# Kernel optimization log

Hardware: AMD Instinct MI355X
Metric: run time of the kernel (lower is better)

The kernel has to match this reference:

```python
import jax, jax.numpy as jnp
import numpy as np

DIM = 512; NH = 8; HD = DIM // NH; WS = 28; N = WS * WS; H3 = (DIM * 4) // 3; EPS = 1e-6; B = 16


def _rel_pos_index(H, W):
    # static numpy computation of Swin-style relative position index [N, N]
    coords = np.stack(np.meshgrid(np.arange(H), np.arange(W), indexing='ij')).reshape(2, -1)
    rel = (coords[:, :, None] - coords[:, None, :]).transpose(1, 2, 0)
    rel[..., 0] += H - 1
    rel[..., 1] += W - 1
    rel[..., 0] *= 2 * W - 1
    return rel.sum(-1)

RPI = jnp.asarray(_rel_pos_index(WS, WS))  # [N, N] int


def adaptive_ln(x, w, b, a1w, a1b, a2w, a2b):
    # x: [B,C,H,W]; adapt params from global-avg-pooled 1x1 convs (== matmuls)
    C = x.shape[1]
    pooled = x.mean(axis=(2, 3))                      # [B,C]
    h = jax.nn.relu(pooled @ a1w.T + a1b)             # [B,C/4]
    ad = h @ a2w.T + a2b                              # [B,2C]
    aw = ad[:, :C][:, :, None, None]
    ab = ad[:, C:][:, :, None, None]
    u = x.mean(axis=1, keepdims=True)
    s = ((x - u) ** 2).mean(axis=1, keepdims=True)
    xn = (x - u) * jax.lax.rsqrt(s + EPS)
    return (w[None, :, None, None] * (1.0 + aw)) * xn + (b[None, :, None, None] + ab)


def dwconv(x, w, b):
    y = jax.lax.conv_general_dilated(x, w, (1, 1), 'SAME', feature_group_count=x.shape[1],
                                     dimension_numbers=('NCHW', 'OIHW', 'NCHW'))
    return y + b[None, :, None, None]


def conv1x1(x, w, b):
    return jnp.einsum('bchw,oc->bohw', x, w) + b[None, :, None, None]


def _forward(x, face_priors, n1_w, n1_b, n1_a1w, n1_a1b, n1_a2w, n1_a2b,
             n2_w, n2_b, n2_a1w, n2_a1b, n2_a2w, n2_a2b,
             qkv_w, qkv_b, rpb_table, struct_prior, proj_w, proj_b,
             eye_w, eye_b, nose_w, nose_b, mouth_w, mouth_b,
             fusion_w, fusion_b, gate1_w, gate1_b, gate2_w, gate2_b,
             es1_w, es1_b, es2_w, es2_b, em1_w, em1_b, em2_w, em2_b,
             el1_w, el1_b, el2_w, el2_b, router_w, router_b):
    Bx, C, H, W = x.shape
    n = H * W
    shortcut = x
    xa = adaptive_ln(x, n1_w, n1_b, n1_a1w, n1_a1b, n1_a2w, n1_a2b)
    # --- TripletFaceAttention ---
    xf = xa.reshape(Bx, C, n).transpose(0, 2, 1)                     # [B,N,C]
    qkv = (xf @ qkv_w.T + qkv_b).reshape(Bx, n, 3, NH, HD).transpose(2, 0, 3, 1, 4)
    q, k, v = qkv[0], qkv[1], qkv[2]                                 # [B,h,N,d]
    attn = jnp.einsum('bhnd,bhmd->bhnm', q, k) * (HD ** -0.5)
    attn = attn + struct_prior                                       # learned structure prior [1,h,N,N]
    rpb = rpb_table[RPI]                                             # [N,N,h]
    attn = attn + jnp.transpose(rpb, (2, 0, 1))[None]                # + relative position bias
    attn = attn * face_priors[:, None]                               # multiplicative face mask
    attn = jax.nn.softmax(attn, axis=-1)
    o = jnp.einsum('bhnm,bhmd->bhnd', attn, v).transpose(0, 2, 1, 3).reshape(Bx, n, C)
    o = o @ proj_w.T + proj_b
    x = shortcut + o.transpose(0, 2, 1).reshape(Bx, C, H, W)
    # --- FaceTokenMixer ---
    xn2 = adaptive_ln(x, n2_w, n2_b, n2_a1w, n2_a1b, n2_a2w, n2_a2b)
    cat = jnp.concatenate([dwconv(xn2, eye_w, eye_b),
                           dwconv(xn2, nose_w, nose_b),
                           dwconv(xn2, mouth_w, mouth_b)], axis=1)   # [B,3C,H,W]
    g = jax.nn.sigmoid(conv1x1(jax.nn.relu(conv1x1(xn2, gate1_w, gate1_b)), gate2_w, gate2_b))
    x = x + conv1x1(cat * g, fusion_w, fusion_b)
    # --- EfficientMLP (3-expert MoE, soft routing) ---
    r = jax.nn.softmax(x.mean(axis=(2, 3)) @ router_w.T + router_b, axis=-1)  # [B,3]
    def expert(w1, b1, w2, b2):
        return conv1x1(jax.nn.gelu(conv1x1(x, w1, b1), approximate=False), w2, b2)
    out = (r[:, 0, None, None, None] * expert(es1_w, es1_b, es2_w, es2_b)
           + r[:, 1, None, None, None] * expert(em1_w, em1_b, em2_w, em2_b)
           + r[:, 2, None, None, None] * expert(el1_w, el1_b, el2_w, el2_b))
    return x + out


def setup_inputs() -> dict:
    ks = iter(jax.random.split(jax.random.key(0), 64))
    def rn(shape, s=0.02):
        return jax.random.normal(next(ks), shape, jnp.float32) * s
    d = {}
    d['x'] = jax.random.normal(next(ks), (B, DIM, WS, WS), jnp.float32)
    d['face_priors'] = jax.random.uniform(next(ks), (B, N, N), jnp.float32)
    for p in ('n1', 'n2'):
        d[p + '_w'] = jnp.ones((DIM,), jnp.float32)
        d[p + '_b'] = jnp.zeros((DIM,), jnp.float32)
        d[p + '_a1w'] = rn((DIM // 4, DIM)); d[p + '_a1b'] = jnp.zeros((DIM // 4,), jnp.float32)
        d[p + '_a2w'] = rn((2 * DIM, DIM // 4)); d[p + '_a2b'] = jnp.zeros((2 * DIM,), jnp.float32)
    d['qkv_w'] = rn((3 * DIM, DIM)); d['qkv_b'] = jnp.zeros((3 * DIM,), jnp.float32)
    d['rpb_table'] = rn(((2 * WS - 1) ** 2, NH))
    d['struct_prior'] = rn((1, NH, N, N))
    d['proj_w'] = rn((DIM, DIM)); d['proj_b'] = jnp.zeros((DIM,), jnp.float32)
    d['eye_w'] = rn((DIM, 1, 3, 3)); d['eye_b'] = jnp.zeros((DIM,), jnp.float32)
    d['nose_w'] = rn((DIM, 1, 5, 5)); d['nose_b'] = jnp.zeros((DIM,), jnp.float32)
    d['mouth_w'] = rn((DIM, 1, 7, 7)); d['mouth_b'] = jnp.zeros((DIM,), jnp.float32)
    d['fusion_w'] = rn((DIM, 3 * DIM)); d['fusion_b'] = jnp.zeros((DIM,), jnp.float32)
    d['gate1_w'] = rn((DIM // 4, DIM)); d['gate1_b'] = jnp.zeros((DIM // 4,), jnp.float32)
    d['gate2_w'] = rn((3 * DIM, DIM // 4)); d['gate2_b'] = jnp.zeros((3 * DIM,), jnp.float32)
    for e in ('es', 'em', 'el'):
        d[e + '1_w'] = rn((H3, DIM)); d[e + '1_b'] = jnp.zeros((H3,), jnp.float32)
        d[e + '2_w'] = rn((DIM, H3)); d[e + '2_b'] = jnp.zeros((DIM,), jnp.float32)
    d['router_w'] = rn((3, DIM)); d['router_b'] = jnp.zeros((3,), jnp.float32)
    return d


def reference(x, face_priors, n1_w, n1_b, n1_a1w, n1_a1b, n1_a2w, n1_a2b,
              n2_w, n2_b, n2_a1w, n2_a1b, n2_a2w, n2_a2b,
              qkv_w, qkv_b, rpb_table, struct_prior, proj_w, proj_b,
              eye_w, eye_b, nose_w, nose_b, mouth_w, mouth_b,
              fusion_w, fusion_b, gate1_w, gate1_b, gate2_w, gate2_b,
              es1_w, es1_b, es2_w, es2_b, em1_w, em1_b, em2_w, em2_b,
              el1_w, el1_b, el2_w, el2_b, router_w, router_b):
    return _forward(x, face_priors, n1_w, n1_b, n1_a1w, n1_a1b, n1_a2w, n1_a2b,
                    n2_w, n2_b, n2_a1w, n2_a1b, n2_a2w, n2_a2b,
                    qkv_w, qkv_b, rpb_table, struct_prior, proj_w, proj_b,
                    eye_w, eye_b, nose_w, nose_b, mouth_w, mouth_b,
                    fusion_w, fusion_b, gate1_w, gate1_b, gate2_w, gate2_b,
                    es1_w, es1_b, es2_w, es2_b, em1_w, em1_b, em2_w, em2_b,
                    el1_w, el1_b, el2_w, el2_b, router_w, router_b)
```

## Files before the change

### kernel.cpp

```cpp
#include <hip/hip_runtime.h>
#include <math.h>


#define NPIX 784
#define CDIM 512
#define NHEAD 8
#define C3 1536

typedef unsigned int uint;
typedef unsigned short ushort;
typedef float f32x4 __attribute__((ext_vector_type(4)));
typedef __bf16 bf16x8 __attribute__((ext_vector_type(8)));
typedef __bf16 bf16x2 __attribute__((ext_vector_type(2)));

#define OFF_XPM ((size_t)0)
#define OFF_W   ((size_t)3211264)
#define OFF_R2  ((size_t)5324288)
#define OFF_VBF ((size_t)14958080)
#define OFF_OBF ((size_t)18169344)
#define OFF_X2  ((size_t)21380608)
#define OFF_X3  ((size_t)27803136)
#define OFF_PL  ((size_t)34225664)
#define OFF_AD  ((size_t)34233856)
#define OFF_RB  ((size_t)34250240)
#define OFF_US  ((size_t)34250288)
#define OFF_RS  ((size_t)34262832)
#define OFF_E2C ((size_t)34275392)

#define WOFF_QKV 0
#define WOFF_PROJ 786432
#define WOFF_G1  1048576
#define WOFF_G2  1114112
#define WOFF_FUS 1310720
#define WOFF_E1  2097152

__device__ __forceinline__ ushort f2bf(float f) {
  __bf16 h = (__bf16)f;
  return __builtin_bit_cast(ushort, h);
}
__device__ __forceinline__ unsigned pack2bf(float lo, float hi) {
  bf16x2 v = {(__bf16)lo, (__bf16)hi};
  return __builtin_bit_cast(unsigned, v);
}
__device__ __forceinline__ float bf2f(ushort u) {
  unsigned x = ((unsigned)u) << 16;
  return __builtin_bit_cast(float, x);
}
__device__ __forceinline__ void unpack4bf(uint2 v, float* o) {
  o[0] = bf2f((ushort)(v.x & 0xffffu)); o[1] = bf2f((ushort)(v.x >> 16));
  o[2] = bf2f((ushort)(v.y & 0xffffu)); o[3] = bf2f((ushort)(v.y >> 16));
}

__global__ __launch_bounds__(64) void pool_mean_k(const float* __restrict__ x,
                                                  float* __restrict__ pooled) {
  int c = blockIdx.x, b = blockIdx.y;
  const float* row = x + ((size_t)b * CDIM + c) * NPIX;
  float s = 0.f;
  for (int i = threadIdx.x; i < NPIX; i += 64) s += row[i];
  #pragma unroll
  for (int off = 32; off; off >>= 1) s += __shfl_down(s, off);
  if (threadIdx.x == 0) pooled[b * CDIM + c] = s;
}

__global__ __launch_bounds__(256) void adapt_mlp_k(const float* __restrict__ pooled,
                                                   const float* __restrict__ a1w,
                                                   const float* __restrict__ a1b,
                                                   const float* __restrict__ a2w,
                                                   const float* __restrict__ a2b,
                                                   float* __restrict__ ad) {
  int b = blockIdx.x, tid = threadIdx.x;
  __shared__ float pl[CDIM];
  __shared__ float hh[128];
  for (int i = tid; i < CDIM; i += 256)
    pl[i] = pooled[b * CDIM + i] * (1.f / NPIX);
  __syncthreads();
  if (tid < 128) {
    const float* w = a1w + (size_t)tid * CDIM;
    float a = a1b[tid];
    for (int k = 0; k < CDIM; ++k) a += w[k] * pl[k];
    hh[tid] = fmaxf(a, 0.f);
  }
  __syncthreads();
  for (int o = tid; o < 1024; o += 256) {
    const float* w = a2w + (size_t)o * 128;
    float a = a2b[o];
    for (int k = 0; k < 128; ++k) a += w[k] * hh[k];
    ad[b * 1024 + o] = a;
  }
}

template <int STATS>
__global__ __launch_bounds__(256) void ln_pm_k(const float* __restrict__ x,
                                               const float* __restrict__ w,
                                               const float* __restrict__ bias,
                                               const float* __restrict__ ad,
                                               ushort* __restrict__ out,
                                               float* __restrict__ ust,
                                               float* __restrict__ rstp) {
  int b = blockIdx.y;
  int p0 = blockIdx.x * 32;
  int tid = threadIdx.x;
  int px = tid & 31, cg = tid >> 5;
  int p = p0 + px;
  bool valid = p < NPIX;
  const float* xb = x + (size_t)b * CDIM * NPIX;
  float s = 0.f, s2 = 0.f;
  if (valid) {
    for (int c = cg * 64; c < cg * 64 + 64; ++c) {
      float v = xb[(size_t)c * NPIX + p];
      s += v; s2 += v * v;
    }
  }
  __shared__ float rs[8][32], rq[8][32], us[32], vs[32];
  rs[cg][px] = s; rq[cg][px] = s2;
  __syncthreads();
  if (tid < 32) {
    float ts = 0.f, ts2 = 0.f;
    #pragma unroll
    for (int g = 0; g < 8; ++g) { ts += rs[g][tid]; ts2 += rq[g][tid]; }
    float u = ts * (1.f / CDIM);
    float var = ts2 * (1.f / CDIM) - u * u;
    float rv = rsqrtf(var + 1e-6f);
    us[tid] = u; vs[tid] = rv;
    if (STATS && p0 + tid < NPIX) {
      ust[(size_t)b * NPIX + p0 + tid] = u;
      rstp[(size_t)b * NPIX + p0 + tid] = rv;
    }
  }
  __syncthreads();
  if (valid) {
    float u = us[px], rv = vs[px];
    const float* aw = ad + (size_t)b * 1024;
    const float* ab = aw + CDIM;
    ushort* ob = out + ((size_t)(b * NPIX + p)) * CDIM + cg * 64;
    for (int cb = 0; cb < 64; cb += 8) {
      int c = cg * 64 + cb;
      float vv[8];
      #pragma unroll
      for (int q = 0; q < 8; ++q) {
        float v = xb[(size_t)(c + q) * NPIX + p];
        vv[q] = w[c + q] * (1.f + aw[c + q]) * ((v - u) * rv) + (bias[c + q] + ab[c + q]);
      }
      uint4 o = {pack2bf(vv[0], vv[1]), pack2bf(vv[2], vv[3]),
                 pack2bf(vv[4], vv[5]), pack2bf(vv[6], vv[7])};
      *(uint4*)(ob + cb) = o;
    }
  }
}

struct CvtDesc {
  const float* s[11];
  ushort* d[11];
  int rows[11], sk[11], dk[11], ds[11], rr[11];
};
__global__ __launch_bounds__(256) void cvt_w_k(CvtDesc D) {
  int seg = blockIdx.y;
  int sk = D.sk[seg], dk = D.dk[seg], ds = D.ds[seg], rr = D.rr[seg];
  int total = D.rows[seg] * dk;
  const float* s = D.s[seg];
  ushort* d = D.d[seg];
  for (int i = blockIdx.x * 256 + threadIdx.x; i < total; i += gridDim.x * 256) {
    int r = i / dk, cc = i - r * dk;
    d[(size_t)r * ds + cc] = (cc < sk && r < rr) ? f2bf(s[(size_t)r * sk + cc]) : (ushort)0;
  }
}

__global__ __launch_bounds__(256) void sprpb_k(const float* __restrict__ sp,
                                               const float* __restrict__ rpb,
                                               ushort* __restrict__ out) {
  const int q = blockIdx.x, h = blockIdx.y;
  const int i1 = q / 28, j1 = q - i1 * 28;
  const float* src = sp + ((size_t)h * NPIX + q) * NPIX;
  ushort* dst = out + ((size_t)h * NPIX + q) * NPIX;
  for (int m = threadIdx.x; m < NPIX; m += 256) {
    int i2 = m / 28, j2 = m - i2 * 28;
    float rv = rpb[(size_t)((i1 - i2 + 27) * 55 + (j1 - j2 + 27)) * NHEAD + h];
    dst[m] = f2bf(src[m] + rv);
  }
}

__global__ __launch_bounds__(256) void fpcvt_k(const float* __restrict__ fp,
                                               ushort* __restrict__ out) {
  size_t i = (size_t)blockIdx.x * 256 + threadIdx.x;
  float4 v = *((const float4*)fp + i);
  ushort4 o;
  o.x = f2bf(v.x); o.y = f2bf(v.y); o.z = f2bf(v.z); o.w = f2bf(v.w);
  *((ushort4*)out + i) = o;
}

__global__ __launch_bounds__(512) void biaseff_k(const float* __restrict__ rbuf,
                                                 const float* __restrict__ b0,
                                                 const float* __restrict__ b1,
                                                 const float* __restrict__ b2,
                                                 const float* __restrict__ a0,
                                                 const float* __restrict__ a1,
                                                 const float* __restrict__ a2,
                                                 float* __restrict__ be,
                                                 float* __restrict__ e1bcat) {
  int b = blockIdx.x;
  if (b < 16) {
    int n = threadIdx.x;
    be[b * 512 + n] = rbuf[b * 3] * b0[n] + rbuf[b * 3 + 1] * b1[n] + rbuf[b * 3 + 2] * b2[n];
  } else {
    for (int i = threadIdx.x; i < 2112; i += 512) {
      int e = i / 704, r = i - e * 704;
      e1bcat[i] = (r < 682) ? (e == 0 ? a0 : e == 1 ? a1 : a2)[r] : 0.f;
    }
  }
}

template <int ORIENT, int EPI, int POOL, int DUALBF, int BN>
__global__ __launch_bounds__(256) void mgemm_k(const ushort* __restrict__ X,
                                               const ushort* __restrict__ Wt,
                                               const float* __restrict__ bias,
                                               const float* __restrict__ resid,
                                               const float* __restrict__ scales,
                                               void* __restrict__ OutV,
                                               float* __restrict__ pool_out,
                                               ushort* __restrict__ pm_out,
                                               int Ks, int Nreal, int Nstore) {
  constexpr int NFRAG = BN / 64;
  const int bid = blockIdx.x;
  const int xcd = bid & 7;
  const int i = bid >> 3;
  const int mt_local = i % 14;
  const int nt = i / 14;
  const int m0 = (xcd * 14 + mt_local) * 112;
  const int n0 = nt * BN;
  const int bb = m0 / NPIX;
  const int t = threadIdx.x;
  const int w = t >> 6, lane = t & 63, c = lane & 15, g = lane >> 4;
  __shared__ ushort Xs[7168];
  __shared__ ushort Ws[BN * 64];
  f32x4 acc[7][NFRAG];
  #pragma unroll
  for (int mi = 0; mi < 7; ++mi)
    #pragma unroll
    for (int ni = 0; ni < NFRAG; ++ni) acc[mi][ni] = (f32x4){0.f, 0.f, 0.f, 0.f};

  for (int k0 = 0; k0 < Ks; k0 += 64) {
    for (int ii = t; ii < 896; ii += 256) {
      int m = ii >> 3, kg = ii & 7;
      uint4 v = *(const uint4*)(X + (size_t)(m0 + m) * Ks + k0 + kg * 8);
      *(uint4*)&Xs[m * 64 + ((kg ^ (m & 7)) << 3)] = v;
    }
    for (int ii = t; ii < BN * 8; ii += 256) {
      int n = ii >> 3, kg = ii & 7;
      uint4 v = {0u, 0u, 0u, 0u};
      if (n0 + n < Nreal) v = *(const uint4*)(Wt + (size_t)(n0 + n) * Ks + k0 + kg * 8);
      *(uint4*)&Ws[n * 64 + ((kg ^ (n & 7)) << 3)] = v;
    }
    __syncthreads();
    #pragma unroll
    for (int kc = 0; kc < 2; ++kc) {
      bf16x8 xf[7], wf[NFRAG];
      #pragma unroll
      for (int mi = 0; mi < 7; ++mi) {
        int m = mi * 16 + c;
        xf[mi] = *(const bf16x8*)&Xs[m * 64 + (((kc * 4 + g) ^ (m & 7)) << 3)];
      }
      #pragma unroll
      for (int ni = 0; ni < NFRAG; ++ni) {
        int n = w * (16 * NFRAG) + ni * 16 + c;
        wf[ni] = *(const bf16x8*)&Ws[n * 64 + (((kc * 4 + g) ^ (n & 7)) << 3)];
      }
      #pragma unroll
      for (int mi = 0; mi < 7; ++mi)
        #pragma unroll
        for (int ni = 0; ni < NFRAG; ++ni)
          acc[mi][ni] = (ORIENT == 0)
            ? __builtin_amdgcn_mfma_f32_16x16x32_bf16(wf[ni], xf[mi], acc[mi][ni], 0, 0, 0)
            : __builtin_amdgcn_mfma_f32_16x16x32_bf16(xf[mi], wf[ni], acc[mi][ni], 0, 0, 0);
    }
    __syncthreads();
  }

  if (ORIENT == 0) {
    ushort* Ob = (ushort*)OutV;
    const int nbq = n0 + w * (16 * NFRAG);
    float bi[NFRAG][4];
    #pragma unroll
    for (int ni = 0; ni < NFRAG; ++ni)
      #pragma unroll
      for (int j = 0; j < 4; ++j) {
        int n = nbq + ni * 16 + g * 4 + j;
        bi[ni][j] = (n < Nreal) ? bias[n] : 0.f;
      }
    #pragma unroll
    for (int mi = 0; mi < 7; ++mi) {
      int m = m0 + mi * 16 + c;
      #pragma unroll
      for (int ni = 0; ni < NFRAG; ++ni) {
        int nb = nbq + ni * 16 + g * 4;
        if (nb >= Nstore) continue;
        float v[4];
        #pragma unroll
        for (int j = 0; j < 4; ++j) v[j] = acc[mi][ni][j] + bi[ni][j];
        if (EPI == 1) {
          #pragma unroll
          for (int j = 0; j < 4; ++j) v[j] = fmaxf(v[j], 0.f);
        } else if (EPI == 2) {
          #pragma unroll
          for (int j = 0; j < 4; ++j)
            v[j] = 0.5f * v[j] * (1.f + erff(v[j] * 0.70710678118654752f));
        } else if (EPI == 3) {
          uint2 cm = *(const uint2*)&Ob[(size_t)m * Nstore + nb];
          float cf[4];
          unpack4bf(cm, cf);
          #pragma unroll
          for (int j = 0; j < 4; ++j)
            v[j] = (1.f / (1.f + __expf(-v[j]))) * cf[j];
        } else if (EPI == 5) {
          int e = nb / 704; e = (e > 2) ? 2 : e;
          float sc = scales[bb * 3 + e];
          #pragma unroll
          for (int j = 0; j < 4; ++j)
            v[j] = 0.5f * v[j] * (1.f + erff(v[j] * 0.70710678118654752f)) * sc;
        }
        uint2 o = {pack2bf(v[0], v[1]), pack2bf(v[2], v[3])};
        *(uint2*)&Ob[(size_t)m * Nstore + nb] = o;
      }
    }
  } else {
    const int prow = m0 - bb * NPIX;
    float* Ob = (float*)OutV + (size_t)bb * CDIM * NPIX;
    const float* Rb = resid + (size_t)bb * CDIM * NPIX;
    float sc = (EPI == 4 && scales) ? scales[bb * 3] : 1.f;
    #pragma unroll
    for (int ni = 0; ni < NFRAG; ++ni) {
      int n = n0 + w * (16 * NFRAG) + ni * 16 + c;
      float bv = (EPI == 5) ? bias[(size_t)bb * CDIM + n] : bias[n];
      float cs = 0.f;
      #pragma unroll
      for (int mi = 0; mi < 7; ++mi) {
        int p = prow + mi * 16 + g * 4;
        size_t off = (size_t)n * NPIX + p;
        float4 r = *(const float4*)&Rb[off];
        f32x4 a = acc[mi][ni];
        float4 o = {r.x + sc * (a[0] + bv), r.y + sc * (a[1] + bv),
                    r.z + sc * (a[2] + bv), r.w + sc * (a[3] + bv)};
        *(float4*)&Ob[off] = o;
        if (POOL) cs += o.x + o.y + o.z + o.w;
        if (DUALBF) {
          size_t mg = (size_t)(m0 + mi * 16 + g * 4);
          pm_out[mg * CDIM + n] = f2bf(o.x);
          pm_out[(mg + 1) * CDIM + n] = f2bf(o.y);
          pm_out[(mg + 2) * CDIM + n] = f2bf(o.z);
          pm_out[(mg + 3) * CDIM + n] = f2bf(o.w);
        }
      }
      if (POOL) {
        cs += __shfl_xor(cs, 16);
        cs += __shfl_xor(cs, 32);
        if (g == 0) atomicAdd(pool_out + (size_t)bb * CDIM + n, cs);
      }
    }
  }
}

__global__ __launch_bounds__(256) void vtr_k(const ushort* __restrict__ qkvbf,
                                             ushort* __restrict__ vbf) {
  const int p0 = blockIdx.x * 64, c0 = blockIdx.y * 64, b = blockIdx.z;
  __shared__ ushort T[64][72];
  for (int idx = threadIdx.x; idx < 512; idx += 256) {
    int pl = idx >> 3, cq = idx & 7;
    int p = p0 + pl;
    uint4 v = {0u, 0u, 0u, 0u};
    if (p < NPIX)
      v = *(const uint4*)(qkvbf + (size_t)(b * NPIX + p) * C3 + 1024 + c0 + cq * 8);
    *(uint4*)&T[pl][cq * 8] = v;
  }
  __syncthreads();
  for (int idx = threadIdx.x; idx < 512; idx += 256) {
    int cl = idx >> 3, pq = idx & 7;
    if (p0 + pq * 8 < NPIX) {
      ushort tmp[8];
      #pragma unroll
      for (int i = 0; i < 8; ++i) tmp[i] = T[pq * 8 + i][cl];
      *(uint4*)(vbf + ((size_t)(b * CDIM + c0 + cl)) * NPIX + p0 + pq * 8) =
          *(const uint4*)&tmp[0];
    }
  }
}

struct KFr { bf16x8 a0, a1, b0, b1; };
struct VFr { bf16x8 v0, v1, v2, v3; };
struct BFr { uint2 sl, fl, sh, fh; };

__global__ __launch_bounds__(256) void attn_mfma_k(const ushort* __restrict__ qkvbf,
                                                   const ushort* __restrict__ vbf,
                                                   const ushort* __restrict__ sprpb,
                                                   const ushort* __restrict__ fpb,
                                                   ushort* __restrict__ obf) {
  const int bid = blockIdx.x;
  const int xcd = bid & 7;
  const int i = bid >> 3;
  const int b = xcd + 8 * (i / 56);
  const int r = i % 56;
  const int h = r & 7;
  const int qt = r >> 3;
  const int w = threadIdx.x >> 6, lane = threadIdx.x & 63;
  const int g = lane >> 4, c = lane & 15;
  const int q0 = qt * 128 + w * 32;
  if (q0 >= NPIX) return;
  const bool hasB = (q0 + 16) < NPIX;
  const int qA = q0 + c;
  const int qB = q0 + 16 + c;

  __shared__ uint BL[4][2][384];
  uint* bwA = BL[w][0];
  uint* bwB = BL[w][1];

  const ushort* qpA = qkvbf + (size_t)(b * NPIX + qA) * C3 + h * 64 + g * 8;
  const bf16x8 qfA0 = *(const bf16x8*)qpA;
  const bf16x8 qfA1 = *(const bf16x8*)(qpA + 32);
  bf16x8 qfB0 = qfA0, qfB1 = qfA1;
  if (hasB) {
    const ushort* qpB = qkvbf + (size_t)(b * NPIX + qB) * C3 + h * 64 + g * 8;
    qfB0 = *(const bf16x8*)qpB;
    qfB1 = *(const bf16x8*)(qpB + 32);
  }

  const ushort* kbase = qkvbf + (size_t)b * NPIX * C3 + 512 + h * 64 + g * 8;
  const ushort* vbase = vbf + ((size_t)b * CDIM + h * 64) * NPIX;
  const ushort* sprA = sprpb + ((size_t)h * NPIX + qA) * NPIX;
  const ushort* sprB = sprpb + ((size_t)h * NPIX + (hasB ? qB : qA)) * NPIX;
  const ushort* fpA = fpb + ((size_t)b * NPIX + qA) * NPIX;
  const ushort* fpB = fpb + ((size_t)b * NPIX + (hasB ? qB : qA)) * NPIX;

  auto load_k = [&](int m0, bool tfull) -> KFr {
    KFr k;
    const ushort* kp = kbase + (size_t)(m0 + c) * C3;
    k.a0 = *(const bf16x8*)kp;
    k.a1 = *(const bf16x8*)(kp + 32);
    const ushort* kp1 = kp + (tfull ? (size_t)16 * C3 : 0);
    k.b0 = *(const bf16x8*)kp1;
    k.b1 = *(const bf16x8*)(kp1 + 32);
    return k;
  };
  auto load_v = [&](int m0) -> VFr {
    VFr v;
    const ushort* vp = vbase + (size_t)c * NPIX + m0 + g * 8;
    v.v0 = *(const bf16x8*)(vp);
    v.v1 = *(const bf16x8*)(vp + (size_t)16 * NPIX);
    v.v2 = *(const bf16x8*)(vp + (size_t)32 * NPIX);
    v.v3 = *(const bf16x8*)(vp + (size_t)48 * NPIX);
    return v;
  };
  auto load_b = [&](const ushort* spr, const ushort* fp, int m0) -> BFr {
    BFr x;
    x.sl = *(const uint2*)(spr + m0 + g * 4);
    x.fl = *(const uint2*)(fp + m0 + g * 4);
    x.sh = *(const uint2*)(spr + m0 + 16 + g * 4);
    x.fh = *(const uint2*)(fp + m0 + 16 + g * 4);
    return x;
  };

  f32x4 oA0 = {0.f, 0.f, 0.f, 0.f}, oA1 = oA0, oA2 = oA0, oA3 = oA0;
  f32x4 oB0 = oA0, oB1 = oA0, oB2 = oA0, oB3 = oA0;
  float MA = -1e30f, LA = 0.f, MB = -1e30f, LB = 0.f;

  KFr kc = load_k(0, true);
  VFr vc = load_v(0);
  BFr bcA = load_b(sprA, fpA, 0);
  BFr bcB = bcA;
  if (hasB) bcB = load_b(sprB, fpB, 0);

  for (int ms = 0; ms < 25; ++ms) {
    const int m0 = ms * 32;
    const bool full = (ms < 24);

    KFr kn; VFr vn; BFr bnA, bnB;
    if (full) {
      const int nm0 = m0 + 32;
      kn = load_k(nm0, ms + 1 < 24);
      vn = load_v(nm0);
      bnA = load_b(sprA, fpA, nm0);
      if (hasB) bnB = load_b(sprB, fpB, nm0);
    }

    f32x4 sA0 = {0.f, 0.f, 0.f, 0.f}, sA1 = sA0;
    sA0 = __builtin_amdgcn_mfma_f32_16x16x32_bf16(kc.a0, qfA0, sA0, 0, 0, 0);
    sA0 = __builtin_amdgcn_mfma_f32_16x16x32_bf16(kc.a1, qfA1, sA0, 0, 0, 0);
    if (full) {
      sA1 = __builtin_amdgcn_mfma_f32_16x16x32_bf16(kc.b0, qfA0, sA1, 0, 0, 0);
      sA1 = __builtin_amdgcn_mfma_f32_16x16x32_bf16(kc.b1, qfA1, sA1, 0, 0, 0);
    }
    {
      float vA0[4], vA1[4];
      float spv[4], fpv[4];
      unpack4bf(bcA.sl, spv);
      unpack4bf(bcA.fl, fpv);
      #pragma unroll
      for (int j = 0; j < 4; ++j) vA0[j] = fmaf(sA0[j], 0.125f, spv[j]) * fpv[j];
      if (full) {
        unpack4bf(bcA.sh, spv);
        unpack4bf(bcA.fh, fpv);
        #pragma unroll
        for (int j = 0; j < 4; ++j) vA1[j] = fmaf(sA1[j], 0.125f, spv[j]) * fpv[j];
      }
      float tm = fmaxf(fmaxf(vA0[0], vA0[1]), fmaxf(vA0[2], vA0[3]));
      if (full) tm = fmaxf(tm, fmaxf(fmaxf(vA1[0], vA1[1]), fmaxf(vA1[2], vA1[3])));
      tm = fmaxf(tm, __shfl_xor(tm, 16));
      tm = fmaxf(tm, __shfl_xor(tm, 32));
      if (__any(tm > MA)) {
        const float nM = fmaxf(MA, tm);
        const float fac = __expf(MA - nM);
        LA *= fac;
        #pragma unroll
        for (int j = 0; j < 4; ++j) { oA0[j] *= fac; oA1[j] *= fac; oA2[j] *= fac; oA3[j] *= fac; }
        MA = nM;
      }
      float p0v[4], p1v[4];
      float ps = 0.f;
      #pragma unroll
      for (int j = 0; j < 4; ++j) { p0v[j] = __expf(vA0[j] - MA); ps += p0v[j]; }
      if (full) {
        #pragma unroll
        for (int j = 0; j < 4; ++j) { p1v[j] = __expf(vA1[j] - MA); ps += p1v[j]; }
      }
      ps += __shfl_xor(ps, 16);
      ps += __shfl_xor(ps, 32);
      LA += ps;
      uint2 wlo, whi;
      wlo.x = pack2bf(p0v[0], p0v[1]);
      wlo.y = pack2bf(p0v[2], p0v[3]);
      whi.x = full ? pack2bf(p1v[0], p1v[1]) : 0u;
      whi.y = full ? pack2bf(p1v[2], p1v[3]) : 0u;
      *(uint2*)&bwA[lane * 6] = wlo;
      *(uint2*)&bwA[lane * 6 + 2] = whi;
    }

    if (hasB) {
      f32x4 sB0 = {0.f, 0.f, 0.f, 0.f}, sB1 = sB0;
      sB0 = __builtin_amdgcn_mfma_f32_16x16x32_bf16(kc.a0, qfB0, sB0, 0, 0, 0);
      sB0 = __builtin_amdgcn_mfma_f32_16x16x32_bf16(kc.a1, qfB1, sB0, 0, 0, 0);
      if (full) {
        sB1 = __builtin_amdgcn_mfma_f32_16x16x32_bf16(kc.b0, qfB0, sB1, 0, 0, 0);
        sB1 = __builtin_amdgcn_mfma_f32_16x16x32_bf16(kc.b1, qfB1, sB1, 0, 0, 0);
      }
      float vB0[4], vB1[4];
      float spv[4], fpv[4];
      unpack4bf(bcB.sl, spv);
      unpack4bf(bcB.fl, fpv);
      #pragma unroll
      for (int j = 0; j < 4; ++j) vB0[j] = fmaf(sB0[j], 0.125f, spv[j]) * fpv[j];
      if (full) {
        unpack4bf(bcB.sh, spv);
        unpack4bf(bcB.fh, fpv);
        #pragma unroll
        for (int j = 0; j < 4; ++j) vB1[j] = fmaf(sB1[j], 0.125f, spv[j]) * fpv[j];
      }
      float tm = fmaxf(fmaxf(vB0[0], vB0[1]), fmaxf(vB0[2], vB0[3]));
      if (full) tm = fmaxf(tm, fmaxf(fmaxf(vB1[0], vB1[1]), fmaxf(vB1[2], vB1[3])));
      tm = fmaxf(tm, __shfl_xor(tm, 16));
      tm = fmaxf(tm, __shfl_xor(tm, 32));
      if (__any(tm > MB)) {
        const float nM = fmaxf(MB, tm);
        const float fac = __expf(MB - nM);
        LB *= fac;
        #pragma unroll
        for (int j = 0; j < 4; ++j) { oB0[j] *= fac; oB1[j] *= fac; oB2[j] *= fac; oB3[j] *= fac; }
        MB = nM;
      }
      float p0v[4], p1v[4];
      float ps = 0.f;
      #pragma unroll
      for (int j = 0; j < 4; ++j) { p0v[j] = __expf(vB0[j] - MB); ps += p0v[j]; }
      if (full) {
        #pragma unroll
        for (int j = 0; j < 4; ++j) { p1v[j] = __expf(vB1[j] - MB); ps += p1v[j]; }
      }
      ps += __shfl_xor(ps, 16);
      ps += __shfl_xor(ps, 32);
      LB += ps;
      uint2 wlo, whi;
      wlo.x = pack2bf(p0v[0], p0v[1]);
      wlo.y = pack2bf(p0v[2], p0v[3]);
      whi.x = full ? pack2bf(p1v[0], p1v[1]) : 0u;
      whi.y = full ? pack2bf(p1v[2], p1v[3]) : 0u;
      *(uint2*)&bwB[lane * 6] = wlo;
      *(uint2*)&bwB[lane * 6 + 2] = whi;
    }

    const int f = g >> 1;
    const int slo = 32 * (g & 1) + c;
    uint2 blo = *(const uint2*)&bwA[slo * 6 + f * 2];
    uint2 bhi = *(const uint2*)&bwA[(slo + 16) * 6 + f * 2];
    uint4 bba = {blo.x, blo.y, bhi.x, bhi.y};
    const bf16x8 pfA = __builtin_bit_cast(bf16x8, bba);
    oA0 = __builtin_amdgcn_mfma_f32_16x16x32_bf16(vc.v0, pfA, oA0, 0, 0, 0);
    oA1 = __builtin_amdgcn_mfma_f32_16x16x32_bf16(vc.v1, pfA, oA1, 0, 0, 0);
    oA2 = __builtin_amdgcn_mfma_f32_16x16x32_bf16(vc.v2, pfA, oA2, 0, 0, 0);
    oA3 = __builtin_amdgcn_mfma_f32_16x16x32_bf16(vc.v3, pfA, oA3, 0, 0, 0);
    if (hasB) {
      uint2 clo = *(const uint2*)&bwB[slo * 6 + f * 2];
      uint2 chi = *(const uint2*)&bwB[(slo + 16) * 6 + f * 2];
      uint4 bbb = {clo.x, clo.y, chi.x, chi.y};
      const bf16x8 pfB = __builtin_bit_cast(bf16x8, bbb);
      oB0 = __builtin_amdgcn_mfma_f32_16x16x32_bf16(vc.v0, pfB, oB0, 0, 0, 0);
      oB1 = __builtin_amdgcn_mfma_f32_16x16x32_bf16(vc.v1, pfB, oB1, 0, 0, 0);
      oB2 = __builtin_amdgcn_mfma_f32_16x16x32_bf16(vc.v2, pfB, oB2, 0, 0, 0);
      oB3 = __builtin_amdgcn_mfma_f32_16x16x32_bf16(vc.v3, pfB, oB3, 0, 0, 0);
    }

    if (full) { kc = kn; vc = vn; bcA = bnA; if (hasB) bcB = bnB; }
  }

  {
    const float invL = 1.f / LA;
    ushort* dst = obf + (size_t)(b * NPIX + qA) * CDIM + h * 64 + g * 4;
    f32x4 ot[4] = {oA0, oA1, oA2, oA3};
    #pragma unroll
    for (int t2 = 0; t2 < 4; ++t2) {
      uint2 o = {pack2bf(ot[t2][0] * invL, ot[t2][1] * invL),
                 pack2bf(ot[t2][2] * invL, ot[t2][3] * invL)};
      *(uint2*)(dst + t2 * 16) = o;
    }
  }
  if (hasB) {
    const float invL = 1.f / LB;
    ushort* dst = obf + (size_t)(b * NPIX + qB) * CDIM + h * 64 + g * 4;
    f32x4 ot[4] = {oB0, oB1, oB2, oB3};
    #pragma unroll
    for (int t2 = 0; t2 < 4; ++t2) {
      uint2 o = {pack2bf(ot[t2][0] * invL, ot[t2][1] * invL),
                 pack2bf(ot[t2][2] * invL, ot[t2][3] * invL)};
      *(uint2*)(dst + t2 * 16) = o;
    }
  }
}

__device__ __forceinline__ float bf2f_s(ushort u) { return bf2f(u); }

template <int R>
__device__ __forceinline__ void conv_pass(const ushort* __restrict__ plane_ci,
                                          const float* __restrict__ wl_ci,
                                          float bv, int slot,
                                          ushort (*__restrict__ outb)[16], int ci) {
  constexpr int K = 2 * R + 1;
  float wreg[K * K];
  #pragma unroll
  for (int i = 0; i < K * K; ++i) wreg[i] = wl_ci[i];
  #pragma unroll
  for (int r7 = 0; r7 < 7; ++r7) {
    const int run = slot + r7 * 16;
    const int y = run >> 2, x0 = (run & 3) * 7;
    float acc[7];
    #pragma unroll
    for (int i = 0; i < 7; ++i) acc[i] = bv;
    #pragma unroll
    for (int dy = 0; dy < K; ++dy) {
      const ushort* rp = plane_ci + (y + 3 - R + dy) * 34 + (x0 + 3 - R);
      float win[7 + 2 * R];
      #pragma unroll
      for (int k = 0; k < 7 + 2 * R; ++k) win[k] = bf2f_s(rp[k]);
      #pragma unroll
      for (int i = 0; i < 7; ++i)
        #pragma unroll
        for (int k = 0; k < K; ++k)
          acc[i] = fmaf(win[i + k], wreg[dy * K + k], acc[i]);
    }
    #pragma unroll
    for (int i = 0; i < 7; ++i) outb[y * 28 + x0 + i][ci] = f2bf(acc[i]);
  }
}

__global__ __launch_bounds__(256) void dwln_k(const float* __restrict__ x2,
    const float* __restrict__ ust, const float* __restrict__ rst,
    const float* __restrict__ ad, const float* __restrict__ n2w,
    const float* __restrict__ n2b,
    const float* __restrict__ ew, const float* __restrict__ eb,
    const float* __restrict__ nw, const float* __restrict__ nb,
    const float* __restrict__ mw, const float* __restrict__ mb,
    ushort* __restrict__ cat) {
  const int cg = blockIdx.x, b = blockIdx.y;
  const int c0 = cg * 16;
  const int t = threadIdx.x;
  const int ci = t & 15, slot = t >> 4;

  __shared__ ushort plane[16][1156];
  __shared__ ushort outb[784][16];
  __shared__ float Wl[16 * 49];
  __shared__ float LWs[16], LBs[16];

  {
    uint* pz = (uint*)&plane[0][0];
    for (int i = t; i < 16 * 1156 / 2; i += 256) pz[i] = 0u;
  }
  if (t < 16) {
    int cc = c0 + t;
    float aw = ad[b * 1024 + cc], ab = ad[b * 1024 + 512 + cc];
    LWs[t] = n2w[cc] * (1.f + aw);
    LBs[t] = n2b[cc] + ab;
  }
  __syncthreads();

  {
    float uu[4], rr[4];
    #pragma unroll
    for (int j = 0; j < 4; ++j) {
      int p = t + j * 256;
      if (p < NPIX) {
        uu[j] = ust[(size_t)b * NPIX + p];
        rr[j] = rst[(size_t)b * NPIX + p];
      }
    }
    for (int cc = 0; cc < 16; ++cc) {
      const float* xp = x2 + ((size_t)(b * CDIM + c0 + cc)) * NPIX;
      float lw = LWs[cc], lb = LBs[cc];
      #pragma unroll
      for (int j = 0; j < 4; ++j) {
        int p = t + j * 256;
        if (p < NPIX) {
          int y = p / 28, xx2 = p - y * 28;
          plane[cc][(y + 3) * 34 + xx2 + 3] = f2bf(lw * (xp[p] - uu[j]) * rr[j] + lb);
        }
      }
    }
  }
  __syncthreads();

  #pragma unroll 1
  for (int cv = 0; cv < 3; ++cv) {
    const float* gw = (cv == 0) ? ew : (cv == 1) ? nw : mw;
    const float* gb = (cv == 0) ? eb : (cv == 1) ? nb : mb;
    const int K2 = (cv == 0) ? 9 : (cv == 1) ? 25 : 49;
    for (int i = t; i < 16 * K2; i += 256) {
      int cc = i / K2, k = i - cc * K2;
      Wl[cc * K2 + k] = gw[(size_t)(c0 + cc) * K2 + k];
    }
    __syncthreads();
    float bv = gb[c0 + ci];
    if (cv == 0)      conv_pass<1>(&plane[ci][0], &Wl[ci * 9],  bv, slot, outb, ci);
    else if (cv == 1) conv_pass<2>(&plane[ci][0], &Wl[ci * 25], bv, slot, outb, ci);
    else              conv_pass<3>(&plane[ci][0], &Wl[ci * 49], bv, slot, outb, ci);
    __syncthreads();
    for (int idx = t; idx < NPIX * 2; idx += 256) {
      int p = idx >> 1, half = idx & 1;
      uint4 v = *(const uint4*)&outb[p][half * 8];
      *(uint4*)(cat + ((size_t)(b * NPIX + p)) * C3 + cv * 512 + c0 + half * 8) = v;
    }
    __syncthreads();
  }
}

__global__ __launch_bounds__(64) void router_k(const float* __restrict__ pooled,
                                               const float* __restrict__ rw,
                                               const float* __restrict__ rb,
                                               float* __restrict__ r) {
  int b = blockIdx.x, lane = threadIdx.x;
  float a0 = 0.f, a1 = 0.f, a2 = 0.f;
  for (int k = lane; k < CDIM; k += 64) {
    float p = pooled[b * CDIM + k] * (1.f / NPIX);
    a0 += rw[k] * p;
    a1 += rw[CDIM + k] * p;
    a2 += rw[2 * CDIM + k] * p;
  }
  #pragma unroll
  for (int off = 32; off; off >>= 1) {
    a0 += __shfl_down(a0, off);
    a1 += __shfl_down(a1, off);
    a2 += __shfl_down(a2, off);
  }
  if (lane == 0) {
    float l0 = a0 + rb[0], l1 = a1 + rb[1], l2 = a2 + rb[2];
    float mx = fmaxf(l0, fmaxf(l1, l2));
    float e0 = __expf(l0 - mx), e1 = __expf(l1 - mx), e2 = __expf(l2 - mx);
    float inv = 1.f / (e0 + e1 + e2);
    r[b * 3 + 0] = e0 * inv;
    r[b * 3 + 1] = e1 * inv;
    r[b * 3 + 2] = e2 * inv;
  }
}

extern "C" void kernel_launch(void* const* d_in, const int* in_sizes, int n_in,
                              void* d_out, int out_size, void* d_ws, size_t ws_size,
                              hipStream_t stream) {
  (void)in_sizes; (void)n_in; (void)out_size; (void)ws_size;
  const float* x         = (const float*)d_in[0];
  const float* fpri      = (const float*)d_in[1];
  const float* n1_w      = (const float*)d_in[2];
  const float* n1_b      = (const float*)d_in[3];
  const float* n1_a1w    = (const float*)d_in[4];
  const float* n1_a1b    = (const float*)d_in[5];
  const float* n1_a2w    = (const float*)d_in[6];
  const float* n1_a2b    = (const float*)d_in[7];
  const float* n2_w      = (const float*)d_in[8];
  const float* n2_b      = (const float*)d_in[9];
  const float* n2_a1w    = (const float*)d_in[10];
  const float* n2_a1b    = (const float*)d_in[11];
  const float* n2_a2w    = (const float*)d_in[12];
  const float* n2_a2b    = (const float*)d_in[13];
  const float* qkv_w     = (const float*)d_in[14];
  const float* qkv_b     = (const float*)d_in[15];
  const float* rpb_table = (const float*)d_in[16];
  const float* sprior    = (const float*)d_in[17];
  const float* proj_w    = (const float*)d_in[18];
  const float* proj_b    = (const float*)d_in[19];
  const float* eye_w     = (const float*)d_in[20];
  const float* eye_b     = (const float*)d_in[21];
  const float* nose_w    = (const float*)d_in[22];
  const float* nose_b    = (const float*)d_in[23];
  const float* mouth_w   = (const float*)d_in[24];
  const float* mouth_b   = (const float*)d_in[25];
  const float* fusion_w  = (const float*)d_in[26];
  const float* fusion_b  = (const float*)d_in[27];
  const float* gate1_w   = (const float*)d_in[28];
  const float* gate1_b   = (const float*)d_in[29];
  const float* gate2_w   = (const float*)d_in[30];
  const float* gate2_b   = (const float*)d_in[31];
  const float* e1w[3] = {(const float*)d_in[32], (const float*)d_in[36], (const float*)d_in[40]};
  const float* e1b[3] = {(const float*)d_in[33], (const float*)d_in[37], (const float*)d_in[41]};
  const float* e2w[3] = {(const float*)d_in[34], (const float*)d_in[38], (const float*)d_in[42]};
  const float* e2b[3] = {(const float*)d_in[35], (const float*)d_in[39], (const float*)d_in[43]};
  const float* router_w  = (const float*)d_in[44];
  const float* router_b  = (const float*)d_in[45];

  float* ws    = (float*)d_ws;
  ushort* xpm  = (ushort*)(ws + OFF_XPM);
  ushort* wb   = (ushort*)(ws + OFF_W);
  ushort* r2u  = (ushort*)(ws + OFF_R2);
  ushort* vbf  = (ushort*)(ws + OFF_VBF);
  ushort* obf  = (ushort*)(ws + OFF_OBF);
  float* x2    = ws + OFF_X2;
  float* x3    = ws + OFF_X3;
  float* pld   = ws + OFF_PL;
  float* adb   = ws + OFF_AD;
  float* rbuf  = ws + OFF_RB;
  float* ust   = ws + OFF_US;
  float* rst   = ws + OFF_RS;
  float* outp  = (float*)d_out;

  ushort* qkvw  = wb + WOFF_QKV;
  ushort* projw = wb + WOFF_PROJ;
  ushort* g1w   = wb + WOFF_G1;
  ushort* g2w   = wb + WOFF_G2;
  ushort* fusw  = wb + WOFF_FUS;
  ushort* e1cat = wb + WOFF_E1;
  ushort* e2cat = (ushort*)(ws + OFF_E2C);
  float* be     = adb;
  float* e1bcat = adb + 8192;

  ushort* fpbf   = (ushort*)x2;
  ushort* sprpbf = (ushort*)x3;

  CvtDesc D;
  auto seg = [&](int s2, const float* src, ushort* dst, int rows, int sk, int dk,
                 int ds, int rr) {
    D.s[s2] = src; D.d[s2] = dst; D.rows[s2] = rows; D.sk[s2] = sk;
    D.dk[s2] = dk; D.ds[s2] = ds; D.rr[s2] = rr;
  };
  seg(0, qkv_w,    qkvw,  1536, 512,  512,  512,  1536);
  seg(1, proj_w,   projw, 512,  512,  512,  512,  512);
  seg(2, gate1_w,  g1w,   128,  512,  512,  512,  128);
  seg(3, gate2_w,  g2w,   1536, 128,  128,  128,  1536);
  seg(4, fusion_w, fusw,  512,  1536, 1536, 1536, 512);
  for (int e = 0; e < 3; ++e) {
    seg(5 + e, e1w[e], e1cat + (size_t)e * 704 * 512, 704, 512, 512, 512, 682);
    seg(8 + e, e2w[e], e2cat + (size_t)e * 704,       512, 682, 704, 2112, 512);
  }
  cvt_w_k<<<dim3(512, 11), 256, 0, stream>>>(D);

  sprpb_k<<<dim3(NPIX, NHEAD), 256, 0, stream>>>(sprior, rpb_table, sprpbf);
  fpcvt_k<<<9604, 256, 0, stream>>>(fpri, fpbf);

  pool_mean_k<<<dim3(CDIM, 16), 64, 0, stream>>>(x, pld);
  adapt_mlp_k<<<16, 256, 0, stream>>>(pld, n1_a1w, n1_a1b, n1_a2w, n1_a2b, adb);
  ln_pm_k<0><<<dim3(25, 16), 256, 0, stream>>>(x, n1_w, n1_b, adb, xpm, nullptr, nullptr);

  mgemm_k<0, 0, 0, 0, 128><<<1344, 256, 0, stream>>>(xpm, qkvw, qkv_b, nullptr, nullptr,
                                                     r2u, nullptr, nullptr, 512, 1536, 1536);
  vtr_k<<<dim3(13, 8, 16), 256, 0, stream>>>(r2u, vbf);
  attn_mfma_k<<<896, 256, 0, stream>>>(r2u, vbf, sprpbf, fpbf, obf);
  hipMemsetAsync(pld, 0, 16 * CDIM * sizeof(float), stream);
  mgemm_k<1, 4, 1, 0, 64><<<896, 256, 0, stream>>>(obf, projw, proj_b, x, nullptr,
                                                   x2, pld, nullptr, 512, 512, 512);

  adapt_mlp_k<<<16, 256, 0, stream>>>(pld, n2_a1w, n2_a1b, n2_a2w, n2_a2b, adb);
  ln_pm_k<1><<<dim3(25, 16), 256, 0, stream>>>(x2, n2_w, n2_b, adb, xpm, ust, rst);
  dwln_k<<<dim3(32, 16), 256, 0, stream>>>(x2, ust, rst, adb, n2_w, n2_b,
                                           eye_w, eye_b, nose_w, nose_b, mouth_w, mouth_b,
                                           r2u);
  mgemm_k<0, 1, 0, 0, 64><<<224, 256, 0, stream>>>(xpm, g1w, gate1_b, nullptr, nullptr,
                                                   obf, nullptr, nullptr, 512, 128, 128);
  mgemm_k<0, 3, 0, 0, 128><<<1344, 256, 0, stream>>>(obf, g2w, gate2_b, nullptr, nullptr,
                                                     r2u, nullptr, nullptr, 128, 1536, 1536);
  hipMemsetAsync(pld, 0, 16 * CDIM * sizeof(float), stream);
  mgemm_k<1, 4, 1, 1, 64><<<896, 256, 0, stream>>>(r2u, fusw, fusion_b, x2, nullptr,
                                                   x3, pld, xpm, 1536, 512, 512);

  router_k<<<16, 64, 0, stream>>>(pld, router_w, router_b, rbuf);
  biaseff_k<<<17, 512, 0, stream>>>(rbuf, e2b[0], e2b[1], e2b[2],
                                    e1b[0], e1b[1], e1b[2], be, e1bcat);
  mgemm_k<0, 5, 0, 0, 128><<<1904, 256, 0, stream>>>(xpm, e1cat, e1bcat, nullptr, rbuf,
                                                     r2u, nullptr, nullptr, 512, 2112, 2112);
  mgemm_k<1, 5, 0, 0, 64><<<896, 256, 0, stream>>>(r2u, e2cat, be, x3, nullptr,
                                                   outp, nullptr, nullptr, 2112, 512, 512);
}
```

Before: 724.1 us.

## Split attention waves to one 16-query tile and use exp2 softmax

The attention kernel now gives each wave a single 16-query tile instead of two. The grid grows from 896 to 1664 blocks, which raises parallelism and lowers per-wave register pressure. The log2(e) factor is folded into the precomputed structural-prior bias and into the score scale, so the softmax can use the native exp2 instruction. MFMA sections are wrapped in s_setprio hints. The cost is that K and V fragments are loaded from memory twice as often per query, which increases memory and cache traffic.

Result: slower. 772.4 us (+6.7%).

```diff
diff --git a/kernel.cpp b/kernel.cpp
--- a/kernel.cpp
+++ b/kernel.cpp
@@ -12,6 +12,9 @@
 typedef float f32x4 __attribute__((ext_vector_type(4)));
 typedef __bf16 bf16x8 __attribute__((ext_vector_type(8)));
 typedef __bf16 bf16x2 __attribute__((ext_vector_type(2)));
+
+#define LOG2E 1.4426950408889634f
+#define KSCL  0.18033688011112042f
 
 #define OFF_XPM ((size_t)0)
 #define OFF_W   ((size_t)3211264)
@@ -175,7 +178,7 @@
   for (int m = threadIdx.x; m < NPIX; m += 256) {
     int i2 = m / 28, j2 = m - i2 * 28;
     float rv = rpb[(size_t)((i1 - i2 + 27) * 55 + (j1 - j2 + 27)) * NHEAD + h];
-    dst[m] = f2bf(src[m] + rv);
+    dst[m] = f2bf((src[m] + rv) * LOG2E);
   }
 }
 
@@ -395,38 +398,27 @@
   const int bid = blockIdx.x;
   const int xcd = bid & 7;
   const int i = bid >> 3;
-  const int b = xcd + 8 * (i / 56);
-  const int r = i % 56;
+  const int b = xcd + 8 * (i / 104);
+  const int r = i % 104;
   const int h = r & 7;
   const int qt = r >> 3;
   const int w = threadIdx.x >> 6, lane = threadIdx.x & 63;
   const int g = lane >> 4, c = lane & 15;
-  const int q0 = qt * 128 + w * 32;
-  if (q0 >= NPIX) return;
-  const bool hasB = (q0 + 16) < NPIX;
-  const int qA = q0 + c;
-  const int qB = q0 + 16 + c;
-
-  __shared__ uint BL[4][2][384];
-  uint* bwA = BL[w][0];
-  uint* bwB = BL[w][1];
-
-  const ushort* qpA = qkvbf + (size_t)(b * NPIX + qA) * C3 + h * 64 + g * 8;
-  const bf16x8 qfA0 = *(const bf16x8*)qpA;
-  const bf16x8 qfA1 = *(const bf16x8*)(qpA + 32);
-  bf16x8 qfB0 = qfA0, qfB1 = qfA1;
-  if (hasB) {
-    const ushort* qpB = qkvbf + (size_t)(b * NPIX + qB) * C3 + h * 64 + g * 8;
-    qfB0 = *(const bf16x8*)qpB;
-    qfB1 = *(const bf16x8*)(qpB + 32);
-  }
+  const int q0 = qt * 64 + w * 16;
+  if (q0 + 16 > NPIX) return;
+  const int q = q0 + c;
+
+  __shared__ uint BL[4][384];
+  uint* bw = BL[w];
+
+  const ushort* qp = qkvbf + (size_t)(b * NPIX + q) * C3 + h * 64 + g * 8;
+  const bf16x8 qf0 = *(const bf16x8*)qp;
+  const bf16x8 qf1 = *(const bf16x8*)(qp + 32);
 
   const ushort* kbase = qkvbf + (size_t)b * NPIX * C3 + 512 + h * 64 + g * 8;
   const ushort* vbase = vbf + ((size_t)b * CDIM + h * 64) * NPIX;
-  const ushort* sprA = sprpb + ((size_t)h * NPIX + qA) * NPIX;
-  const ushort* sprB = sprpb + ((size_t)h * NPIX + (hasB ? qB : qA)) * NPIX;
-  const ushort* fpA = fpb + ((size_t)b * NPIX + qA) * NPIX;
-  const ushort* fpB = fpb + ((size_t)b * NPIX + (hasB ? qB : qA)) * NPIX;
+  const ushort* spr = sprpb + ((size_t)h * NPIX + q) * NPIX;
+  const ushort* fp = fpb + ((size_t)b * NPIX + q) * NPIX;
 
   auto load_k = [&](int m0, bool tfull) -> KFr {
     KFr k;
@@ -447,7 +439,7 @@
     v.v3 = *(const bf16x8*)(vp + (size_t)48 * NPIX);
     return v;
   };
-  auto load_b = [&](const ushort* spr, const ushort* fp, int m0) -> BFr {
+  auto load_b = [&](int m0) -> BFr {
     BFr x;
     x.sl = *(const uint2*)(spr + m0 + g * 4);
     x.fl = *(const uint2*)(fp + m0 + g * 4);
@@ -456,172 +448,103 @@
     return x;
   };
 
-  f32x4 oA0 = {0.f, 0.f, 0.f, 0.f}, oA1 = oA0, oA2 = oA0, oA3 = oA0;
-  f32x4 oB0 = oA0, oB1 = oA0, oB2 = oA0, oB3 = oA0;
-  float MA = -1e30f, LA = 0.f, MB = -1e30f, LB = 0.f;
+  f32x4 o0 = {0.f, 0.f, 0.f, 0.f}, o1 = o0, o2 = o0, o3 = o0;
+  float M = -1e30f, L = 0.f;
 
   KFr kc = load_k(0, true);
   VFr vc = load_v(0);
-  BFr bcA = load_b(sprA, fpA, 0);
-  BFr bcB = bcA;
-  if (hasB) bcB = load_b(sprB, fpB, 0);
+  BFr bc = load_b(0);
 
   for (int ms = 0; ms < 25; ++ms) {
     const int m0 = ms * 32;
     const bool full = (ms < 24);
 
-    KFr kn; VFr vn; BFr bnA, bnB;
+    KFr kn; VFr vn; BFr bn;
     if (full) {
       const int nm0 = m0 + 32;
       kn = load_k(nm0, ms + 1 < 24);
       vn = load_v(nm0);
-      bnA = load_b(sprA, fpA, nm0);
-      if (hasB) bnB = load_b(sprB, fpB, nm0);
-    }
-
-    f32x4 sA0 = {0.f, 0.f, 0.f, 0.f}, sA1 = sA0;
-    sA0 = __builtin_amdgcn_mfma_f32_16x16x32_bf16(kc.a0, qfA0, sA0, 0, 0, 0);
-    sA0 = __builtin_amdgcn_mfma_f32_16x16x32_bf16(kc.a1, qfA1, sA0, 0, 0, 0);
+      bn = load_b(nm0);
+    }
+
+    f32x4 s0 = {0.f, 0.f, 0.f, 0.f}, s1 = s0;
+    __builtin_amdgcn_s_setprio(1);
+    s0 = __builtin_amdgcn_mfma_f32_16x16x32_bf16(kc.a0, qf0, s0, 0, 0, 0);
+    s0 = __builtin_amdgcn_mfma_f32_16x16x32_bf16(kc.a1, qf1, s0, 0, 0, 0);
     if (full) {
-      sA1 = __builtin_amdgcn_mfma_f32_16x16x32_bf16(kc.b0, qfA0, sA1, 0, 0, 0);
-      sA1 = __builtin_amdgcn_mfma_f32_16x16x32_bf16(kc.b1, qfA1, sA1, 0, 0, 0);
-    }
+      s1 = __builtin_amdgcn_mfma_f32_16x16x32_bf16(kc.b0, qf0, s1, 0, 0, 0);
+      s1 = __builtin_amdgcn_mfma_f32_16x16x32_bf16(kc.b1, qf1, s1, 0, 0, 0);
+    }
+    __builtin_amdgcn_s_setprio(0);
+
+    float v0[4], v1[4];
     {
-      float vA0[4], vA1[4];
       float spv[4], fpv[4];
-      unpack4bf(bcA.sl, spv);
-      unpack4bf(bcA.fl, fpv);
-      #pragma unroll
-      for (int j = 0; j < 4; ++j) vA0[j] = fmaf(sA0[j], 0.125f, spv[j]) * fpv[j];
+      unpack4bf(bc.sl, spv);
+      unpack4bf(bc.fl, fpv);
+      #pragma unroll
+      for (int j = 0; j < 4; ++j) v0[j] = fmaf(s0[j], KSCL, spv[j]) * fpv[j];
       if (full) {
-        unpack4bf(bcA.sh, spv);
-        unpack4bf(bcA.fh, fpv);
+        unpack4bf(bc.sh, spv);
+        unpack4bf(bc.fh, fpv);
         #pragma unroll
-        for (int j = 0; j < 4; ++j) vA1[j] = fmaf(sA1[j], 0.125f, spv[j]) * fpv[j];
-      }
-      float tm = fmaxf(fmaxf(vA0[0], vA0[1]), fmaxf(vA0[2], vA0[3]));
-      if (full) tm = fmaxf(tm, fmaxf(fmaxf(vA1[0], vA1[1]), fmaxf(vA1[2], vA1[3])));
+        for (int j = 0; j < 4; ++j) v1[j] = fmaf(s1[j], KSCL, spv[j]) * fpv[j];
+      }
+    }
+
+    {
+      float tm = fmaxf(fmaxf(v0[0], v0[1]), fmaxf(v0[2], v0[3]));
+      if (full) tm = fmaxf(tm, fmaxf(fmaxf(v1[0], v1[1]), fmaxf(v1[2], v1[3])));
       tm = fmaxf(tm, __shfl_xor(tm, 16));
       tm = fmaxf(tm, __shfl_xor(tm, 32));
-      if (__any(tm > MA)) {
-        const float nM = fmaxf(MA, tm);
-        const float fac = __expf(MA - nM);
-        LA *= fac;
+      if (__any(tm > M)) {
+        const float nM = fmaxf(M, tm);
+        const float fac = __builtin_amdgcn_exp2f(M - nM);
+        L *= fac;
         #pragma unroll
-        for (int j = 0; j < 4; ++j) { oA0[j] *= fac; oA1[j] *= fac; oA2[j] *= fac; oA3[j] *= fac; }
-        MA = nM;
+        for (int j = 0; j < 4; ++j) { o0[j] *= fac; o1[j] *= fac; o2[j] *= fac; o3[j] *= fac; }
+        M = nM;
       }
       float p0v[4], p1v[4];
       float ps = 0.f;
       #pragma unroll
-      for (int j = 0; j < 4; ++j) { p0v[j] = __expf(vA0[j] - MA); ps += p0v[j]; }
+      for (int j = 0; j < 4; ++j) { p0v[j] = __builtin_amdgcn_exp2f(v0[j] - M); ps += p0v[j]; }
       if (full) {
         #pragma unroll
-        for (int j = 0; j < 4; ++j) { p1v[j] = __expf(vA1[j] - MA); ps += p1v[j]; }
+        for (int j = 0; j < 4; ++j) { p1v[j] = __builtin_amdgcn_exp2f(v1[j] - M); ps += p1v[j]; }
       }
       ps += __shfl_xor(ps, 16);
       ps += __shfl_xor(ps, 32);
-      LA += ps;
+      L += ps;
       uint2 wlo, whi;
       wlo.x = pack2bf(p0v[0], p0v[1]);
       wlo.y = pack2bf(p0v[2], p0v[3]);
       whi.x = full ? pack2bf(p1v[0], p1v[1]) : 0u;
       whi.y = full ? pack2bf(p1v[2], p1v[3]) : 0u;
-      *(uint2*)&bwA[lane * 6] = wlo;
-      *(uint2*)&bwA[lane * 6 + 2] = whi;
-    }
-
-    if (hasB) {
-      f32x4 sB0 = {0.f, 0.f, 0.f, 0.f}, sB1 = sB0;
-      sB0 = __builtin_amdgcn_mfma_f32_16x16x32_bf16(kc.a0, qfB0, sB0, 0, 0, 0);
-      sB0 = __builtin_amdgcn_mfma_f32_16x16x32_bf16(kc.a1, qfB1, sB0, 0, 0, 0);
-      if (full) {
-        sB1 = __builtin_amdgcn_mfma_f32_16x16x32_bf16(kc.b0, qfB0, sB1, 0, 0, 0);
-        sB1 = __builtin_amdgcn_mfma_f32_16x16x32_bf16(kc.b1, qfB1, sB1, 0, 0, 0);
-      }
-      float vB0[4], vB1[4];
-      float spv[4], fpv[4];
-      unpack4bf(bcB.sl, spv);
-      unpack4bf(bcB.fl, fpv);
-      #pragma unroll
-      for (int j = 0; j < 4; ++j) vB0[j] = fmaf(sB0[j], 0.125f, spv[j]) * fpv[j];
-      if (full) {
-        unpack4bf(bcB.sh, spv);
-        unpack4bf(bcB.fh, fpv);
-        #pragma unroll
-        for (int j = 0; j < 4; ++j) vB1[j] = fmaf(sB1[j], 0.125f, spv[j]) * fpv[j];
-      }
-      float tm = fmaxf(fmaxf(vB0[0], vB0[1]), fmaxf(vB0[2], vB0[3]));
-      if (full) tm = fmaxf(tm, fmaxf(fmaxf(vB1[0], vB1[1]), fmaxf(vB1[2], vB1[3])));
-      tm = fmaxf(tm, __shfl_xor(tm, 16));
-      tm = fmaxf(tm, __shfl_xor(tm, 32));
-      if (__any(tm > MB)) {
-        const float nM = fmaxf(MB, tm);
-        const float fac = __expf(MB - nM);
-        LB *= fac;
-        #pragma unroll
-        for (int j = 0; j < 4; ++j) { oB0[j] *= fac; oB1[j] *= fac; oB2[j] *= fac; oB3[j] *= fac; }
-        MB = nM;
-      }
-      float p0v[4], p1v[4];
-      float ps = 0.f;
-      #pragma unroll
-      for (int j = 0; j < 4; ++j) { p0v[j] = __expf(vB0[j] - MB); ps += p0v[j]; }
-      if (full) {
-        #pragma unroll
-        for (int j = 0; j < 4; ++j) { p1v[j] = __expf(vB1[j] - MB); ps += p1v[j]; }
-      }
-      ps += __shfl_xor(ps, 16);
-      ps += __shfl_xor(ps, 32);
-      LB += ps;
-      uint2 wlo, whi;
-      wlo.x = pack2bf(p0v[0], p0v[1]);
-      wlo.y = pack2bf(p0v[2], p0v[3]);
-      whi.x = full ? pack2bf(p1v[0], p1v[1]) : 0u;
-      whi.y = full ? pack2bf(p1v[2], p1v[3]) : 0u;
-      *(uint2*)&bwB[lane * 6] = wlo;
-      *(uint2*)&bwB[lane * 6 + 2] = whi;
+      *(uint2*)&bw[lane * 6] = wlo;
+      *(uint2*)&bw[lane * 6 + 2] = whi;
     }
 
     const int f = g >> 1;
     const int slo = 32 * (g & 1) + c;
-    uint2 blo = *(const uint2*)&bwA[slo * 6 + f * 2];
-    uint2 bhi = *(const uint2*)&bwA[(slo + 16) * 6 + f * 2];
+    uint2 blo = *(const uint2*)&bw[slo * 6 + f * 2];
+    uint2 bhi = *(const uint2*)&bw[(slo + 16) * 6 + f * 2];
     uint4 bba = {blo.x, blo.y, bhi.x, bhi.y};
-    const bf16x8 pfA = __builtin_bit_cast(bf16x8, bba);
-    oA0 = __builtin_amdgcn_mfma_f32_16x16x32_bf16(vc.v0, pfA, oA0, 0, 0, 0);
-    oA1 = __builtin_amdgcn_mfma_f32_16x16x32_bf16(vc.v1, pfA, oA1, 0, 0, 0);
-    oA2 = __builtin_amdgcn_mfma_f32_16x16x32_bf16(vc.v2, pfA, oA2, 0, 0, 0);
-    oA3 = __builtin_amdgcn_mfma_f32_16x16x32_bf16(vc.v3, pfA, oA3, 0, 0, 0);
-    if (hasB) {
-      uint2 clo = *(const uint2*)&bwB[slo * 6 + f * 2];
-      uint2 chi = *(const uint2*)&bwB[(slo + 16) * 6 + f * 2];
-      uint4 bbb = {clo.x, clo.y, chi.x, chi.y};
-      const bf16x8 pfB = __builtin_bit_cast(bf16x8, bbb);
-      oB0 = __builtin_amdgcn_mfma_f32_16x16x32_bf16(vc.v0, pfB, oB0, 0, 0, 0);
-      oB1 = __builtin_amdgcn_mfma_f32_16x16x32_bf16(vc.v1, pfB, oB1, 0, 0, 0);
-      oB2 = __builtin_amdgcn_mfma_f32_16x16x32_bf16(vc.v2, pfB, oB2, 0, 0, 0);
-      oB3 = __builtin_amdgcn_mfma_f32_16x16x32_bf16(vc.v3, pfB, oB3, 0, 0, 0);
-    }
-
-    if (full) { kc = kn; vc = vn; bcA = bnA; if (hasB) bcB = bnB; }
+    const bf16x8 pf = __builtin_bit_cast(bf16x8, bba);
+    __builtin_amdgcn_s_setprio(1);
+    o0 = __builtin_amdgcn_mfma_f32_16x16x32_bf16(vc.v0, pf, o0, 0, 0, 0);
+    o1 = __builtin_amdgcn_mfma_f32_16x16x32_bf16(vc.v1, pf, o1, 0, 0, 0);
+    o2 = __builtin_amdgcn_mfma_f32_16x16x32_bf16(vc.v2, pf, o2, 0, 0, 0);
+    o3 = __builtin_amdgcn_mfma_f32_16x16x32_bf16(vc.v3, pf, o3, 0, 0, 0);
+    __builtin_amdgcn_s_setprio(0);
+
+    if (full) { kc = kn; vc = vn; bc = bn; }
   }
 
   {
-    const float invL = 1.f / LA;
-    ushort* dst = obf + (size_t)(b * NPIX + qA) * CDIM + h * 64 + g * 4;
-    f32x4 ot[4] = {oA0, oA1, oA2, oA3};
-    #pragma unroll
-    for (int t2 = 0; t2 < 4; ++t2) {
-      uint2 o = {pack2bf(ot[t2][0] * invL, ot[t2][1] * invL),
-                 pack2bf(ot[t2][2] * invL, ot[t2][3] * invL)};
-      *(uint2*)(dst + t2 * 16) = o;
-    }
-  }
-  if (hasB) {
-    const float invL = 1.f / LB;
-    ushort* dst = obf + (size_t)(b * NPIX + qB) * CDIM + h * 64 + g * 4;
-    f32x4 ot[4] = {oB0, oB1, oB2, oB3};
+    const float invL = 1.f / L;
+    ushort* dst = obf + (size_t)(b * NPIX + q) * CDIM + h * 64 + g * 4;
+    f32x4 ot[4] = {o0, o1, o2, o3};
     #pragma unroll
     for (int t2 = 0; t2 < 4; ++t2) {
       uint2 o = {pack2bf(ot[t2][0] * invL, ot[t2][1] * invL),
@@ -872,7 +795,7 @@
   mgemm_k<0, 0, 0, 0, 128><<<1344, 256, 0, stream>>>(xpm, qkvw, qkv_b, nullptr, nullptr,
                                                      r2u, nullptr, nullptr, 512, 1536, 1536);
   vtr_k<<<dim3(13, 8, 16), 256, 0, stream>>>(r2u, vbf);
-  attn_mfma_k<<<896, 256, 0, stream>>>(r2u, vbf, sprpbf, fpbf, obf);
+  attn_mfma_k<<<1664, 256, 0, stream>>>(r2u, vbf, sprpbf, fpbf, obf);
   hipMemsetAsync(pld, 0, 16 * CDIM * sizeof(float), stream);
   mgemm_k<1, 4, 1, 0, 64><<<896, 256, 0, stream>>>(obf, projw, proj_b, x, nullptr,
                                                    x2, pld, nullptr, 512, 512, 512);
```
